# Kernel optimization log

Measured on AMD Instinct MI355X. Metric: run time of the kernel, lower is better.

Reference implementation:

```python
import jax, jax.numpy as jnp
import numpy as np

KS = 7            # kernel_size
CH = 3            # channels
THRESH = 128      # threshold (0-255 scale)
TOL = 0.2         # tolerance
PAD = KS // 2


def setup_inputs() -> dict:
    key = jax.random.key(0)
    x = jax.random.uniform(key, (16, CH, 1024, 1024), dtype=jnp.float32)
    return {"x": x}


def reference(x):
    # 1) threshold -> binary map
    cond = (x >= THRESH / 255.0).astype(x.dtype)            # [B,C,H,W]
    # 2) reflect pad spatial dims by k//2
    padded = jnp.pad(cond, ((0, 0), (0, 0), (PAD, PAD), (PAD, PAD)), mode='reflect')
    # 3) depthwise box-sum conv (all-ones kernel, groups=C)
    kernel = jnp.ones((CH, 1, KS, KS), dtype=x.dtype)        # OIHW, I=1 per group
    csum = jax.lax.conv_general_dilated(
        padded, kernel,
        window_strides=(1, 1), padding='VALID',
        feature_group_count=CH,
        dimension_numbers=('NCHW', 'OIHW', 'NCHW'))          # [B,C,H,W]
    # 4) tolerance band mask (note: integer floor-div first, matching torch)
    half = KS * KS // 2
    lo = half * TOL
    hi = half * (1.0 - TOL)
    mask = ((csum >= lo) & (csum <= hi)).astype(x.dtype)
    # 5) zero out masked pixels
    return x * (1.0 - mask)
```

## Files before the change

### kernel.cpp

```cpp
#include <hip/hip_runtime.h>


constexpr int H = 1024;
constexpr int W = 1024;
constexpr int BH = 16;
constexpr int NBANDS = H / BH;
constexpr int STEPS = BH + 6;
constexpr int D = 5;

typedef float vfloat4 __attribute__((ext_vector_type(4)));

__device__ __forceinline__ void nt_store4(float* p, float4 v) {
    vfloat4 t;
    t.x = v.x; t.y = v.y; t.z = v.z; t.w = v.w;
    __builtin_nontemporal_store(t, (vfloat4*)p);
}

__device__ __forceinline__ unsigned expand4(unsigned n) {
    unsigned t = (n | (n << 8)) & 0x00FF00FFu;
    return (t | (t << 4)) & 0x0F0F0F0Fu;
}
__device__ __forceinline__ unsigned compress4(unsigned b) {
    unsigned t = (b | (b >> 4)) & 0x00FF00FFu;
    return (t | (t >> 8)) & 0x0000FFFFu;
}

__global__ __launch_bounds__(256, 3)
void backedge_kernel(const float* __restrict__ x, float* __restrict__ out) {
    const int lane = threadIdx.x & 63;
    const int wv   = threadIdx.x >> 6;
    const int band = blockIdx.x * 4 + wv;
    const int n    = blockIdx.y;
    const int r0   = band * BH;
    const float* __restrict__ xi = x   + (size_t)n * (size_t)(H * W);
    float*       __restrict__ oi = out + (size_t)n * (size_t)(H * W);
    const int off = 4 * lane;
    const float THR = 128.0f / 255.0f;

    float4 ring[D][4];
    unsigned int hn[7][2];
#pragma unroll
    for (int i = 0; i < 7; ++i) { hn[i][0] = 0u; hn[i][1] = 0u; }
    unsigned int vs[4] = {0u, 0u, 0u, 0u};

    {
        int g = r0 - 3;
        g = (g < 0) ? -g : g;
        const float* rp = xi + (size_t)g * W;
#pragma unroll
        for (int q = 0; q < 4; ++q)
            ring[0][q] = *(const float4*)(rp + q * 256 + off);
    }

#pragma unroll
    for (int s = 0; s < STEPS; ++s) {
        if (s + 1 < STEPS) {
            int g = r0 - 3 + (s + 1);
            g = (g < 0) ? -g : g;
            g = (g >= H) ? (2 * H - 2 - g) : g;
            const float* rp = xi + (size_t)g * W;
#pragma unroll
            for (int q = 0; q < 4; ++q)
                ring[(s + 1) % D][q] = *(const float4*)(rp + q * 256 + off);
        }

        unsigned int m = 0;
#pragma unroll
        for (int q = 0; q < 4; ++q) {
            const float4 aq = ring[s % D][q];
            m |= ((unsigned)(aq.x >= THR)) << (4 * q + 0);
            m |= ((unsigned)(aq.y >= THR)) << (4 * q + 1);
            m |= ((unsigned)(aq.z >= THR)) << (4 * q + 2);
            m |= ((unsigned)(aq.w >= THR)) << (4 * q + 3);
        }

        const unsigned int up = __shfl_up(m, 1);
        const unsigned int dn = __shfl_down(m, 1);
        const unsigned int hi = __shfl(m, 63);
        const unsigned int lo = __shfl(m, 0);
        const unsigned int SL = (lane == 0) ? (hi << 4) : up;
        const unsigned int SR = (lane == 63) ? (lo >> 4) : dn;

        unsigned int hp[4];
#pragma unroll
        for (int q = 0; q < 4; ++q) {
            unsigned int w = ((SL >> (4 * q + 1)) & 7u)
                           | (((m >> (4 * q)) & 0xFu) << 3)
                           | (((SR >> (4 * q)) & 7u) << 7);
            if (q == 0 && lane == 0) {
                w |= ((m >> 3) & 1u) | (((m >> 2) & 1u) << 1)
                   | (((m >> 1) & 1u) << 2);
            }
            if (q == 3 && lane == 63) {
                w |= (((m >> 14) & 1u) << 7) | (((m >> 13) & 1u) << 8)
                   | (((m >> 12) & 1u) << 9);
            }
            const unsigned int h0 = __popc((w >> 0) & 0x7Fu);
            const unsigned int h1 = __popc((w >> 1) & 0x7Fu);
            const unsigned int h2 = __popc((w >> 2) & 0x7Fu);
            const unsigned int h3 = __popc((w >> 3) & 0x7Fu);
            hp[q] = h0 | (h1 << 8) | (h2 << 16) | (h3 << 24);
        }

        vs[0] += hp[0] - expand4(hn[0][0] & 0xFFFFu);
        vs[1] += hp[1] - expand4(hn[0][0] >> 16);
        vs[2] += hp[2] - expand4(hn[0][1] & 0xFFFFu);
        vs[3] += hp[3] - expand4(hn[0][1] >> 16);
#pragma unroll
        for (int i = 0; i < 6; ++i) {
            hn[i][0] = hn[i + 1][0];
            hn[i][1] = hn[i + 1][1];
        }
        hn[6][0] = compress4(hp[0]) | (compress4(hp[1]) << 16);
        hn[6][1] = compress4(hp[2]) | (compress4(hp[3]) << 16);

        if (s >= 6) {
            const int orow = r0 + s - 6;
            float* op = oi + (size_t)orow * W;
#pragma unroll
            for (int q = 0; q < 4; ++q) {
                const float4 b = ring[(s - 3) % D][q];
                const unsigned int v = vs[q];
                float4 o;
                o.x = ((((v      ) & 0xFFu) - 5u) <= 14u) ? 0.0f : b.x;
                o.y = ((((v >>  8) & 0xFFu) - 5u) <= 14u) ? 0.0f : b.y;
                o.z = ((((v >> 16) & 0xFFu) - 5u) <= 14u) ? 0.0f : b.z;
                o.w = ((((v >> 24)        ) - 5u) <= 14u) ? 0.0f : b.w;
                nt_store4(op + q * 256 + off, o);
            }
        }
    }
}

extern "C" void kernel_launch(void* const* d_in, const int* in_sizes, int n_in,
                              void* d_out, int out_size, void* d_ws, size_t ws_size,
                              hipStream_t stream) {
    const float* x = (const float*)d_in[0];
    float* out = (float*)d_out;
    (void)in_sizes; (void)n_in; (void)d_ws; (void)ws_size; (void)out_size;
    dim3 grid(NBANDS / 4, 16 * 3);
    backedge_kernel<<<grid, dim3(256), 0, stream>>>(x, out);
}
```

Baseline: 352.4 us.

## Partially unroll row loop by ring period and use plain stores

Replaces the fully unrolled 22-step loop with two peeled steps plus a non-unrolled loop whose body is five templated steps, so ring-buffer indices stay compile-time constants. The aim is smaller code and less instruction-cache pressure. It also drops the nontemporal stores for ordinary float4 stores and removes __restrict__ from the image pointers. The loop adds branch overhead, the runtime s checks may remain, and the store-path change could alter cache behaviour for a bandwidth-bound kernel.

```diff
diff --git a/kernel.cpp b/kernel.cpp
--- a/kernel.cpp
+++ b/kernel.cpp
@@ -6,16 +6,11 @@
 constexpr int BH = 16;
 constexpr int NBANDS = H / BH;
 constexpr int STEPS = BH + 6;
-constexpr int D = 5;
 
-typedef float vfloat4 __attribute__((ext_vector_type(4)));
-
-__device__ __forceinline__ void nt_store4(float* p, float4 v) {
-    vfloat4 t;
-    t.x = v.x; t.y = v.y; t.z = v.z; t.w = v.w;
-    __builtin_nontemporal_store(t, (vfloat4*)p);
+__device__ __forceinline__ int reflect_row(int g) {
+    g = (g < 0) ? -g : g;
+    return (g >= H) ? (2 * H - 2 - g) : g;
 }
-
 __device__ __forceinline__ unsigned expand4(unsigned n) {
     unsigned t = (n | (n << 8)) & 0x00FF00FFu;
     return (t | (t << 4)) & 0x0F0F0F0Fu;
@@ -25,6 +20,86 @@
     return (t | (t >> 8)) & 0x0000FFFFu;
 }
 
+template <int CUR>
+__device__ __forceinline__ void do_step(int s, float4 (&ring)[5][4],
+                                        unsigned (&hn)[7][2], unsigned (&vs)[4],
+                                        const float* xi, float* oi,
+                                        int r0, int off, int lane) {
+    constexpr int NXT = (CUR + 1) % 5;
+    constexpr int PQ  = (CUR + 2) % 5;
+
+    if (s + 1 < STEPS) {
+        const float* rp = xi + (size_t)reflect_row(r0 - 3 + s + 1) * W;
+#pragma unroll
+        for (int q = 0; q < 4; ++q)
+            ring[NXT][q] = *(const float4*)(rp + q * 256 + off);
+    }
+
+    const float THR = 128.0f / 255.0f;
+    unsigned m = 0;
+#pragma unroll
+    for (int q = 0; q < 4; ++q) {
+        const float4 aq = ring[CUR][q];
+        m |= ((unsigned)(aq.x >= THR)) << (4 * q + 0);
+        m |= ((unsigned)(aq.y >= THR)) << (4 * q + 1);
+        m |= ((unsigned)(aq.z >= THR)) << (4 * q + 2);
+        m |= ((unsigned)(aq.w >= THR)) << (4 * q + 3);
+    }
+
+    const unsigned up = __shfl_up(m, 1);
+    const unsigned dn = __shfl_down(m, 1);
+    const unsigned hi = __shfl(m, 63);
+    const unsigned lo = __shfl(m, 0);
+    const unsigned SL = (lane == 0) ? (hi << 4) : up;
+    const unsigned SR = (lane == 63) ? (lo >> 4) : dn;
+
+    unsigned hp[4];
+#pragma unroll
+    for (int q = 0; q < 4; ++q) {
+        unsigned w = ((SL >> (4 * q + 1)) & 7u)
+                   | (((m >> (4 * q)) & 0xFu) << 3)
+                   | (((SR >> (4 * q)) & 7u) << 7);
+        if (q == 0 && lane == 0) {
+            w |= ((m >> 3) & 1u) | (((m >> 2) & 1u) << 1) | (((m >> 1) & 1u) << 2);
+        }
+        if (q == 3 && lane == 63) {
+            w |= (((m >> 14) & 1u) << 7) | (((m >> 13) & 1u) << 8) | (((m >> 12) & 1u) << 9);
+        }
+        const unsigned h0 = __popc((w >> 0) & 0x7Fu);
+        const unsigned h1 = __popc((w >> 1) & 0x7Fu);
+        const unsigned h2 = __popc((w >> 2) & 0x7Fu);
+        const unsigned h3 = __popc((w >> 3) & 0x7Fu);
+        hp[q] = h0 | (h1 << 8) | (h2 << 16) | (h3 << 24);
+    }
+
+    vs[0] += hp[0] - expand4(hn[0][0] & 0xFFFFu);
+    vs[1] += hp[1] - expand4(hn[0][0] >> 16);
+    vs[2] += hp[2] - expand4(hn[0][1] & 0xFFFFu);
+    vs[3] += hp[3] - expand4(hn[0][1] >> 16);
+#pragma unroll
+    for (int i = 0; i < 6; ++i) {
+        hn[i][0] = hn[i + 1][0];
+        hn[i][1] = hn[i + 1][1];
+    }
+    hn[6][0] = compress4(hp[0]) | (compress4(hp[1]) << 16);
+    hn[6][1] = compress4(hp[2]) | (compress4(hp[3]) << 16);
+
+    if (s >= 6) {
+        float* op = oi + (size_t)(r0 + s - 6) * W;
+#pragma unroll
+        for (int q = 0; q < 4; ++q) {
+            const float4 b = ring[PQ][q];
+            const unsigned v = vs[q];
+            float4 o;
+            o.x = ((((v      ) & 0xFFu) - 5u) <= 14u) ? 0.0f : b.x;
+            o.y = ((((v >>  8) & 0xFFu) - 5u) <= 14u) ? 0.0f : b.y;
+            o.z = ((((v >> 16) & 0xFFu) - 5u) <= 14u) ? 0.0f : b.z;
+            o.w = ((((v >> 24)        ) - 5u) <= 14u) ? 0.0f : b.w;
+            *(float4*)(op + q * 256 + off) = o;
+        }
+    }
+}
+
 __global__ __launch_bounds__(256, 3)
 void backedge_kernel(const float* __restrict__ x, float* __restrict__ out) {
     const int lane = threadIdx.x & 63;
@@ -32,103 +107,34 @@
     const int band = blockIdx.x * 4 + wv;
     const int n    = blockIdx.y;
     const int r0   = band * BH;
-    const float* __restrict__ xi = x   + (size_t)n * (size_t)(H * W);
-    float*       __restrict__ oi = out + (size_t)n * (size_t)(H * W);
+    const float* xi = x   + (size_t)n * (size_t)(H * W);
+    float*       oi = out + (size_t)n * (size_t)(H * W);
     const int off = 4 * lane;
-    const float THR = 128.0f / 255.0f;
 
-    float4 ring[D][4];
-    unsigned int hn[7][2];
+    float4 ring[5][4];
+    unsigned hn[7][2];
 #pragma unroll
     for (int i = 0; i < 7; ++i) { hn[i][0] = 0u; hn[i][1] = 0u; }
-    unsigned int vs[4] = {0u, 0u, 0u, 0u};
+    unsigned vs[4] = {0u, 0u, 0u, 0u};
 
     {
-        int g = r0 - 3;
-        g = (g < 0) ? -g : g;
-        const float* rp = xi + (size_t)g * W;
+        const float* rp = xi + (size_t)reflect_row(r0 - 3) * W;
 #pragma unroll
         for (int q = 0; q < 4; ++q)
             ring[0][q] = *(const float4*)(rp + q * 256 + off);
     }
 
-#pragma unroll
-    for (int s = 0; s < STEPS; ++s) {
-        if (s + 1 < STEPS) {
-            int g = r0 - 3 + (s + 1);
-            g = (g < 0) ? -g : g;
-            g = (g >= H) ? (2 * H - 2 - g) : g;
-            const float* rp = xi + (size_t)g * W;
-#pragma unroll
-            for (int q = 0; q < 4; ++q)
-                ring[(s + 1) % D][q] = *(const float4*)(rp + q * 256 + off);
-        }
+    do_step<0>(0, ring, hn, vs, xi, oi, r0, off, lane);
+    do_step<1>(1, ring, hn, vs, xi, oi, r0, off, lane);
 
-        unsigned int m = 0;
-#pragma unroll
-        for (int q = 0; q < 4; ++q) {
-            const float4 aq = ring[s % D][q];
-            m |= ((unsigned)(aq.x >= THR)) << (4 * q + 0);
-            m |= ((unsigned)(aq.y >= THR)) << (4 * q + 1);
-            m |= ((unsigned)(aq.z >= THR)) << (4 * q + 2);
-            m |= ((unsigned)(aq.w >= THR)) << (4 * q + 3);
-        }
-
-        const unsigned int up = __shfl_up(m, 1);
-        const unsigned int dn = __shfl_down(m, 1);
-        const unsigned int hi = __shfl(m, 63);
-        const unsigned int lo = __shfl(m, 0);
-        const unsigned int SL = (lane == 0) ? (hi << 4) : up;
-        const unsigned int SR = (lane == 63) ? (lo >> 4) : dn;
-
-        unsigned int hp[4];
-#pragma unroll
-        for (int q = 0; q < 4; ++q) {
-            unsigned int w = ((SL >> (4 * q + 1)) & 7u)
-                           | (((m >> (4 * q)) & 0xFu) << 3)
-                           | (((SR >> (4 * q)) & 7u) << 7);
-            if (q == 0 && lane == 0) {
-                w |= ((m >> 3) & 1u) | (((m >> 2) & 1u) << 1)
-                   | (((m >> 1) & 1u) << 2);
-            }
-            if (q == 3 && lane == 63) {
-                w |= (((m >> 14) & 1u) << 7) | (((m >> 13) & 1u) << 8)
-                   | (((m >> 12) & 1u) << 9);
-            }
-            const unsigned int h0 = __popc((w >> 0) & 0x7Fu);
-            const unsigned int h1 = __popc((w >> 1) & 0x7Fu);
-            const unsigned int h2 = __popc((w >> 2) & 0x7Fu);
-            const unsigned int h3 = __popc((w >> 3) & 0x7Fu);
-            hp[q] = h0 | (h1 << 8) | (h2 << 16) | (h3 << 24);
-        }
-
-        vs[0] += hp[0] - expand4(hn[0][0] & 0xFFFFu);
-        vs[1] += hp[1] - expand4(hn[0][0] >> 16);
-        vs[2] += hp[2] - expand4(hn[0][1] & 0xFFFFu);
-        vs[3] += hp[3] - expand4(hn[0][1] >> 16);
-#pragma unroll
-        for (int i = 0; i < 6; ++i) {
-            hn[i][0] = hn[i + 1][0];
-            hn[i][1] = hn[i + 1][1];
-        }
-        hn[6][0] = compress4(hp[0]) | (compress4(hp[1]) << 16);
-        hn[6][1] = compress4(hp[2]) | (compress4(hp[3]) << 16);
-
-        if (s >= 6) {
-            const int orow = r0 + s - 6;
-            float* op = oi + (size_t)orow * W;
-#pragma unroll
-            for (int q = 0; q < 4; ++q) {
-                const float4 b = ring[(s - 3) % D][q];
-                const unsigned int v = vs[q];
-                float4 o;
-                o.x = ((((v      ) & 0xFFu) - 5u) <= 14u) ? 0.0f : b.x;
-                o.y = ((((v >>  8) & 0xFFu) - 5u) <= 14u) ? 0.0f : b.y;
-                o.z = ((((v >> 16) & 0xFFu) - 5u) <= 14u) ? 0.0f : b.z;
-                o.w = ((((v >> 24)        ) - 5u) <= 14u) ? 0.0f : b.w;
-                nt_store4(op + q * 256 + off, o);
-            }
-        }
+#pragma unroll 1
+    for (int j = 0; j < 4; ++j) {
+        const int s = 2 + 5 * j;
+        do_step<2>(s    , ring, hn, vs, xi, oi, r0, off, lane);
+        do_step<3>(s + 1, ring, hn, vs, xi, oi, r0, off, lane);
+        do_step<4>(s + 2, ring, hn, vs, xi, oi, r0, off, lane);
+        do_step<0>(s + 3, ring, hn, vs, xi, oi, r0, off, lane);
+        do_step<1>(s + 4, ring, hn, vs, xi, oi, r0, off, lane);
     }
 }
 
```

Result: no change. 352.1 us (-0.1%).
